# Kernel tuning notes

Measured on AMD Instinct MI355X. Metric: run time of the kernel, lower is better.

The kernel has to match this reference:

```python
import jax, jax.numpy as jnp
import numpy as np

KAPPA = 5.0
EPS_NORM = 1e-12  # torch F.normalize eps
EPS_LOG = 1e-09


def setup_inputs() -> dict:
    key = jax.random.key(0)
    student_output = jax.random.normal(key, (16384, 256), dtype=jnp.float32)
    return {"student_output": student_output}


def reference(student_output) -> jnp.ndarray:
    # L2-normalize rows (matches F.normalize: x / max(||x||, eps))
    norm = jnp.linalg.norm(student_output, axis=-1, keepdims=True)
    x_norm = student_output / jnp.maximum(norm, EPS_NORM)
    # pairwise cosine similarity [n, n]
    sim = x_norm @ x_norm.T
    kernel = jnp.exp(KAPPA * sim)
    density_estimates = kernel.sum(axis=1)  # [n]
    entropy = -jnp.mean(jnp.log(density_estimates + EPS_LOG))
    return entropy
```

## Files before the change

kernel.cpp:

```cpp
#include <hip/hip_runtime.h>


#define NROWS 16384
#define KDIM 256
#define NTILE 128
#define NT (NROWS / NTILE)
#define NSTRIP 4
#define TOTAL_BLOCKS (NT * NSTRIP)

#define SQRT_KLOG2E 2.68579577857f

typedef int i32x4_t __attribute__((ext_vector_type(4)));
typedef int i32x8_t __attribute__((ext_vector_type(8)));
typedef float f32x2_t __attribute__((ext_vector_type(2)));
typedef float f32x4_t __attribute__((ext_vector_type(4)));
typedef __attribute__((address_space(1))) const void global_cvoid_t;
typedef __attribute__((address_space(3))) void lds_void_t;

#if __has_builtin(__builtin_amdgcn_exp2f)
#define EXP2(x) __builtin_amdgcn_exp2f(x)
#else
#define EXP2(x) exp2f(x)
#endif

union frag32 { i32x8_t v8; i32x4_t v4[2]; };

__global__ __launch_bounds__(256)
void kde_normalize(const float* __restrict__ X, unsigned int* __restrict__ Xn8,
                   float* __restrict__ density, unsigned int* __restrict__ ticket) {
  const int wave = threadIdx.x >> 6;
  const int lane = threadIdx.x & 63;
  const int row = blockIdx.x * 4 + wave;
  const float4 v = ((const float4*)(X + (size_t)row * KDIM))[lane];
  float ss = v.x * v.x + v.y * v.y + v.z * v.z + v.w * v.w;
  ss += __shfl_xor(ss, 1);
  ss += __shfl_xor(ss, 2);
  ss += __shfl_xor(ss, 4);
  ss += __shfl_xor(ss, 8);
  ss += __shfl_xor(ss, 16);
  ss += __shfl_xor(ss, 32);
  const float scale = SQRT_KLOG2E / fmaxf(sqrtf(ss), 1e-12f);
  int p = 0;
  p = __builtin_amdgcn_cvt_pk_fp8_f32(v.x * scale, v.y * scale, p, false);
  p = __builtin_amdgcn_cvt_pk_fp8_f32(v.z * scale, v.w * scale, p, true);
  Xn8[(size_t)row * 64 + lane] = (unsigned int)p;
  if (threadIdx.x < 4) density[blockIdx.x * 4 + threadIdx.x] = 0.0f;
  if (blockIdx.x == 0 && threadIdx.x == 0) *ticket = 0u;
}

__global__ __launch_bounds__(1024, 8)
void kde_gemm(const unsigned char* __restrict__ Xn8, float* __restrict__ density,
              unsigned int* __restrict__ ticket, float* __restrict__ out) {
  extern __shared__ char smem[];
  char* buf0 = smem;
  char* buf1 = smem + 32768;

  const int tid = threadIdx.x;
  const int wave = tid >> 6;
  const int lane = tid & 63;
  const int l16 = lane & 15;
  const int lg = lane >> 4;
  const int wr = wave >> 1;
  const int wc = wave & 1;
  const int m32 = lane & 31;
  const int h = lane >> 5;
  const int bi = blockIdx.x;
  const int s = blockIdx.y;
  const int t0 = s * 16;
  const int nt = (s == 0 && bi < NT / 2) ? 17 : 16;
  const char* Xb = (const char*)Xn8;

#define STAGE(base_row, dst)                                                      \
  for (int c = wave; c < 32; c += 16) {                                           \
    const int rt = c >> 3, kb = (c >> 1) & 3, hh = c & 1;                         \
    const size_t gofs =                                                           \
        (size_t)((base_row) + rt * 32 + m32) * KDIM + kb * 64 + h * 32 + hh * 16; \
    __builtin_amdgcn_global_load_lds((global_cvoid_t*)(Xb + gofs),                \
                                     (lds_void_t*)((dst) + c * 1024), 16, 0, 0);  \
  }

  STAGE(bi * NTILE, buf0);
  STAGE(((bi + t0) & (NT - 1)) * NTILE, buf1);
  __syncthreads();

  const int a_row_off = ((wr >> 1) * 8192) + (((wr & 1) * 16 + l16) * 16);
  const int k_base = ((lg >> 1) * 2048) + ((lg & 1) * 512);
  const int b_base = wc * 16384 + l16 * 16 + k_base;

  frag32 areg[2];
#pragma unroll
  for (int kq = 0; kq < 2; kq++)
#pragma unroll
    for (int p = 0; p < 2; p++)
      areg[kq].v4[p] =
          *(const i32x4_t*)(buf0 + a_row_off + k_base + kq * 4096 + p * 1024);
  __syncthreads();

  f32x2_t rs01 = (f32x2_t)0.0f;
  f32x2_t rs23 = (f32x2_t)0.0f;

  for (int k = 0; k < nt; ++k) {
    const int t = (k == 16) ? 64 : (t0 + k);
    const int J = (bi + t) & (NT - 1);
    char* rbuf = (k & 1) ? buf0 : buf1;
    char* sbuf = (k & 1) ? buf1 : buf0;

    if (k + 1 < nt) {
      const int tn = (k + 1 == 16) ? 64 : (t0 + k + 1);
      STAGE(((bi + tn) & (NT - 1)) * NTILE, sbuf);
    }

    f32x4_t acc[4];
#pragma unroll
    for (int ct = 0; ct < 4; ct++) acc[ct] = (f32x4_t)0.0f;
#pragma unroll
    for (int ct = 0; ct < 4; ct++) {
      const char* pb = rbuf + b_base + (ct >> 1) * 8192 + (ct & 1) * 256;
#pragma unroll
      for (int kq = 0; kq < 2; kq++) {
        frag32 bf;
        bf.v4[0] = *(const i32x4_t*)(pb + kq * 4096);
        bf.v4[1] = *(const i32x4_t*)(pb + kq * 4096 + 1024);
        acc[ct] = __builtin_amdgcn_mfma_scale_f32_16x16x128_f8f6f4(
            areg[kq].v8, bf.v8, acc[ct], 0, 0, 0, 127, 0, 127);
      }
    }

    float cst[4];
#pragma unroll
    for (int ct = 0; ct < 4; ct++) {
      f32x2_t e01, e23;
      e01.x = EXP2(acc[ct][0]);
      e01.y = EXP2(acc[ct][1]);
      e23.x = EXP2(acc[ct][2]);
      e23.y = EXP2(acc[ct][3]);
      rs01 += e01;
      rs23 += e23;
      float cs = (e01.x + e01.y) + (e23.x + e23.y);
      cs += __shfl_xor(cs, 16);
      cs += __shfl_xor(cs, 32);
      cst[ct] = cs;
    }
    if (t != 0) {
      const float v = (lg & 2) ? ((lg & 1) ? cst[3] : cst[2])
                               : ((lg & 1) ? cst[1] : cst[0]);
      atomicAdd(&density[J * NTILE + wc * 64 + lane], v);
    }

    __syncthreads();
  }

  {
    float rsv[4] = {rs01.x, rs01.y, rs23.x, rs23.y};
#pragma unroll
    for (int r = 0; r < 4; r++) {
      float v = rsv[r];
      v += __shfl_xor(v, 1);
      v += __shfl_xor(v, 2);
      v += __shfl_xor(v, 4);
      v += __shfl_xor(v, 8);
      rsv[r] = v;
    }
    const float v = (l16 & 2) ? ((l16 & 1) ? rsv[3] : rsv[2])
                              : ((l16 & 1) ? rsv[1] : rsv[0]);
    if (l16 < 4)
      atomicAdd(&density[bi * NTILE + wr * 16 + lg * 4 + l16], v);
  }
#undef STAGE

  __syncthreads();
  if (tid == 0) {
    __threadfence();
    ((volatile unsigned int*)smem)[0] = atomicAdd(ticket, 1u);
  }
  __syncthreads();
  if (((volatile unsigned int*)smem)[0] == TOTAL_BLOCKS - 1) {
    __threadfence();
    float ssum = 0.0f;
    for (int i = tid; i < NROWS; i += 1024) {
      const float d = __hip_atomic_load(&density[i], __ATOMIC_RELAXED,
                                        __HIP_MEMORY_SCOPE_AGENT);
      ssum += logf(d + 1e-9f);
    }
    ssum += __shfl_xor(ssum, 1);
    ssum += __shfl_xor(ssum, 2);
    ssum += __shfl_xor(ssum, 4);
    ssum += __shfl_xor(ssum, 8);
    ssum += __shfl_xor(ssum, 16);
    ssum += __shfl_xor(ssum, 32);
    float* red = ((float*)smem) + 16;
    if (lane == 0) red[wave] = ssum;
    __syncthreads();
    if (tid == 0) {
      float tot = 0.0f;
      for (int w = 0; w < 16; w++) tot += red[w];
      out[0] = -tot / (float)NROWS;
    }
  }
}

extern "C" void kernel_launch(void* const* d_in, const int* in_sizes, int n_in,
                              void* d_out, int out_size, void* d_ws, size_t ws_size,
                              hipStream_t stream) {
  const float* X = (const float*)d_in[0];
  float* out = (float*)d_out;
  char* ws = (char*)d_ws;
  unsigned int* Xn8 = (unsigned int*)ws;
  float* density = (float*)(ws + (size_t)NROWS * KDIM);
  unsigned int* ticket = (unsigned int*)(density + NROWS);

  hipFuncSetAttribute((const void*)kde_gemm,
                      hipFuncAttributeMaxDynamicSharedMemorySize, 65536);

  kde_normalize<<<NROWS / 4, 256, 0, stream>>>(X, Xn8, density, ticket);
  kde_gemm<<<dim3(NT, NSTRIP), 1024, 65536, stream>>>((const unsigned char*)ws,
                                                      density, ticket, out);
}
```

Baseline: 124.8 us.

## Give each wave private LDS tiles to drop block-wide barriers in GEMM loop

Restructures the fp8 MFMA similarity kernel so each of the 16 waves stages its own 16-column slice of the B tile into a private, XOR-swizzled double buffer. Each wave holds four 16-row A fragments in registers, loaded straight from global memory. Waits are per-wave vmcnt instead of block-wide __syncthreads, and column-sum atomics drop to one per column per wave. In exchange it uses 128KB of LDS and many more registers, so occupancy falls. Each wave also fetches its own B data, and it relies on the global_load_lds ordering being correct.

```diff
diff --git a/kernel.cpp b/kernel.cpp
--- a/kernel.cpp
+++ b/kernel.cpp
@@ -10,6 +10,8 @@
 
 #define SQRT_KLOG2E 2.68579577857f
 
+#define SMEM_BYTES (16 * 8192)
+
 typedef int i32x4_t __attribute__((ext_vector_type(4)));
 typedef int i32x8_t __attribute__((ext_vector_type(8)));
 typedef float f32x2_t __attribute__((ext_vector_type(2)));
@@ -22,6 +24,8 @@
 #else
 #define EXP2(x) exp2f(x)
 #endif
+
+#define WAITVM(n) asm volatile("s_waitcnt vmcnt(" #n ")" ::: "memory")
 
 union frag32 { i32x8_t v8; i32x4_t v4[2]; };
 
@@ -48,125 +52,139 @@
   if (blockIdx.x == 0 && threadIdx.x == 0) *ticket = 0u;
 }
 
-__global__ __launch_bounds__(1024, 8)
+__global__ __launch_bounds__(1024, 4)
 void kde_gemm(const unsigned char* __restrict__ Xn8, float* __restrict__ density,
               unsigned int* __restrict__ ticket, float* __restrict__ out) {
   extern __shared__ char smem[];
-  char* buf0 = smem;
-  char* buf1 = smem + 32768;
 
   const int tid = threadIdx.x;
   const int wave = tid >> 6;
   const int lane = tid & 63;
   const int l16 = lane & 15;
   const int lg = lane >> 4;
-  const int wr = wave >> 1;
-  const int wc = wave & 1;
-  const int m32 = lane & 31;
-  const int h = lane >> 5;
+  const int rg = wave >> 3;
+  const int cg = wave & 7;
   const int bi = blockIdx.x;
   const int s = blockIdx.y;
   const int t0 = s * 16;
   const int nt = (s == 0 && bi < NT / 2) ? 17 : 16;
   const char* Xb = (const char*)Xn8;
 
-#define STAGE(base_row, dst)                                                      \
-  for (int c = wave; c < 32; c += 16) {                                           \
-    const int rt = c >> 3, kb = (c >> 1) & 3, hh = c & 1;                         \
-    const size_t gofs =                                                           \
-        (size_t)((base_row) + rt * 32 + m32) * KDIM + kb * 64 + h * 32 + hh * 16; \
-    __builtin_amdgcn_global_load_lds((global_cvoid_t*)(Xb + gofs),                \
-                                     (lds_void_t*)((dst) + c * 1024), 16, 0, 0);  \
-  }
-
-  STAGE(bi * NTILE, buf0);
-  STAGE(((bi + t0) & (NT - 1)) * NTILE, buf1);
-  __syncthreads();
-
-  const int a_row_off = ((wr >> 1) * 8192) + (((wr & 1) * 16 + l16) * 16);
-  const int k_base = ((lg >> 1) * 2048) + ((lg & 1) * 512);
-  const int b_base = wc * 16384 + l16 * 16 + k_base;
-
-  frag32 areg[2];
+  char* my0 = smem + wave * 8192;
+  char* my1 = my0 + 4096;
+
+  frag32 areg[4][2];
+  {
+    const size_t abase =
+        (size_t)(bi * NTILE + rg * 64 + l16) * KDIM + lg * 32;
+#pragma unroll
+    for (int rt = 0; rt < 4; rt++)
+#pragma unroll
+      for (int kq = 0; kq < 2; kq++)
+#pragma unroll
+        for (int p = 0; p < 2; p++)
+          areg[rt][kq].v4[p] = *(const i32x4_t*)(Xb + abase +
+              (size_t)rt * 16 * KDIM + kq * 128 + p * 16);
+  }
+
+  int stofs[4];
+#pragma unroll
+  for (int i = 0; i < 4; i++) {
+    const int c = i * 4 + lg;
+    stofs[i] = (cg * 16 + c) * KDIM + ((l16 ^ (c & 7)) * 16);
+  }
+
+#define STAGEB(J, dst)                                                    \
+  {                                                                       \
+    const size_t jb = (size_t)(J) * (NTILE * KDIM);                       \
+    _Pragma("unroll")                                                     \
+    for (int i = 0; i < 4; i++)                                           \
+      __builtin_amdgcn_global_load_lds(                                   \
+          (global_cvoid_t*)(Xb + jb + stofs[i]),                          \
+          (lds_void_t*)((dst) + i * 1024), 16, 0, 0);                     \
+  }
+
+  int rdofs[2][2];
 #pragma unroll
   for (int kq = 0; kq < 2; kq++)
 #pragma unroll
     for (int p = 0; p < 2; p++)
-      areg[kq].v4[p] =
-          *(const i32x4_t*)(buf0 + a_row_off + k_base + kq * 4096 + p * 1024);
-  __syncthreads();
-
-  f32x2_t rs01 = (f32x2_t)0.0f;
-  f32x2_t rs23 = (f32x2_t)0.0f;
+      rdofs[kq][p] =
+          l16 * 256 + ((kq * 128 + lg * 32 + p * 16) ^ ((l16 & 7) << 4));
+
+  STAGEB((bi + t0) & (NT - 1), my0);
+  WAITVM(0);
+
+  f32x2_t rs2[8];
+#pragma unroll
+  for (int r = 0; r < 8; r++) rs2[r] = (f32x2_t)0.0f;
 
   for (int k = 0; k < nt; ++k) {
     const int t = (k == 16) ? 64 : (t0 + k);
     const int J = (bi + t) & (NT - 1);
-    char* rbuf = (k & 1) ? buf0 : buf1;
-    char* sbuf = (k & 1) ? buf1 : buf0;
-
-    if (k + 1 < nt) {
+    char* rbuf = (k & 1) ? my1 : my0;
+    char* sbuf = (k & 1) ? my0 : my1;
+    const bool pre = (k + 1 < nt);
+
+    asm volatile("" ::: "memory");
+    if (pre) {
       const int tn = (k + 1 == 16) ? 64 : (t0 + k + 1);
-      STAGE(((bi + tn) & (NT - 1)) * NTILE, sbuf);
+      STAGEB((bi + tn) & (NT - 1), sbuf);
     }
 
     f32x4_t acc[4];
 #pragma unroll
-    for (int ct = 0; ct < 4; ct++) acc[ct] = (f32x4_t)0.0f;
-#pragma unroll
-    for (int ct = 0; ct < 4; ct++) {
-      const char* pb = rbuf + b_base + (ct >> 1) * 8192 + (ct & 1) * 256;
-#pragma unroll
-      for (int kq = 0; kq < 2; kq++) {
-        frag32 bf;
-        bf.v4[0] = *(const i32x4_t*)(pb + kq * 4096);
-        bf.v4[1] = *(const i32x4_t*)(pb + kq * 4096 + 1024);
-        acc[ct] = __builtin_amdgcn_mfma_scale_f32_16x16x128_f8f6f4(
-            areg[kq].v8, bf.v8, acc[ct], 0, 0, 0, 127, 0, 127);
-      }
-    }
-
-    float cst[4];
-#pragma unroll
-    for (int ct = 0; ct < 4; ct++) {
+    for (int rt = 0; rt < 4; rt++) acc[rt] = (f32x4_t)0.0f;
+
+#pragma unroll
+    for (int kq = 0; kq < 2; kq++) {
+      frag32 bf;
+      bf.v4[0] = *(const i32x4_t*)(rbuf + rdofs[kq][0]);
+      bf.v4[1] = *(const i32x4_t*)(rbuf + rdofs[kq][1]);
+#pragma unroll
+      for (int rt = 0; rt < 4; rt++)
+        acc[rt] = __builtin_amdgcn_mfma_scale_f32_16x16x128_f8f6f4(
+            areg[rt][kq].v8, bf.v8, acc[rt], 0, 0, 0, 127, 0, 127);
+    }
+
+    f32x2_t cacc = (f32x2_t)0.0f;
+#pragma unroll
+    for (int rt = 0; rt < 4; rt++) {
       f32x2_t e01, e23;
-      e01.x = EXP2(acc[ct][0]);
-      e01.y = EXP2(acc[ct][1]);
-      e23.x = EXP2(acc[ct][2]);
-      e23.y = EXP2(acc[ct][3]);
-      rs01 += e01;
-      rs23 += e23;
-      float cs = (e01.x + e01.y) + (e23.x + e23.y);
+      e01.x = EXP2(acc[rt][0]);
+      e01.y = EXP2(acc[rt][1]);
+      e23.x = EXP2(acc[rt][2]);
+      e23.y = EXP2(acc[rt][3]);
+      rs2[rt * 2] += e01;
+      rs2[rt * 2 + 1] += e23;
+      cacc += e01;
+      cacc += e23;
+    }
+
+    if (t != 0) {
+      float cs = cacc.x + cacc.y;
       cs += __shfl_xor(cs, 16);
       cs += __shfl_xor(cs, 32);
-      cst[ct] = cs;
-    }
-    if (t != 0) {
-      const float v = (lg & 2) ? ((lg & 1) ? cst[3] : cst[2])
-                               : ((lg & 1) ? cst[1] : cst[0]);
-      atomicAdd(&density[J * NTILE + wc * 64 + lane], v);
-    }
-
-    __syncthreads();
-  }
-
-  {
-    float rsv[4] = {rs01.x, rs01.y, rs23.x, rs23.y};
-#pragma unroll
-    for (int r = 0; r < 4; r++) {
-      float v = rsv[r];
-      v += __shfl_xor(v, 1);
-      v += __shfl_xor(v, 2);
-      v += __shfl_xor(v, 4);
-      v += __shfl_xor(v, 8);
-      rsv[r] = v;
-    }
-    const float v = (l16 & 2) ? ((l16 & 1) ? rsv[3] : rsv[2])
-                              : ((l16 & 1) ? rsv[1] : rsv[0]);
-    if (l16 < 4)
-      atomicAdd(&density[bi * NTILE + wr * 16 + lg * 4 + l16], v);
-  }
-#undef STAGE
+      if (lg == 0) atomicAdd(&density[J * NTILE + cg * 16 + l16], cs);
+      if (pre) WAITVM(1);
+    } else {
+      if (pre) WAITVM(0);
+    }
+  }
+#undef STAGEB
+
+#pragma unroll
+  for (int idx = 0; idx < 16; idx++) {
+    float v = rs2[idx >> 1][idx & 1];
+    v += __shfl_xor(v, 1);
+    v += __shfl_xor(v, 2);
+    v += __shfl_xor(v, 4);
+    v += __shfl_xor(v, 8);
+    if (l16 == 0) {
+      const int rt = idx >> 2, j = idx & 3;
+      atomicAdd(&density[bi * NTILE + rg * 64 + rt * 16 + lg * 4 + j], v);
+    }
+  }
 
   __syncthreads();
   if (tid == 0) {
@@ -210,9 +228,9 @@
   unsigned int* ticket = (unsigned int*)(density + NROWS);
 
   hipFuncSetAttribute((const void*)kde_gemm,
-                      hipFuncAttributeMaxDynamicSharedMemorySize, 65536);
+                      hipFuncAttributeMaxDynamicSharedMemorySize, SMEM_BYTES);
 
   kde_normalize<<<NROWS / 4, 256, 0, stream>>>(X, Xn8, density, ticket);
-  kde_gemm<<<dim3(NT, NSTRIP), 1024, 65536, stream>>>((const unsigned char*)ws,
-                                                      density, ticket, out);
+  kde_gemm<<<dim3(NT, NSTRIP), 1024, SMEM_BYTES, stream>>>(
+      (const unsigned char*)ws, density, ticket, out);
 }
```

After: 137.4 us. 1.1x slower.
